# Kernel optimization log

Hardware: AMD Instinct MI355X
Metric: run time of the kernel (lower is better)

Reference implementation:

```python
import jax, jax.numpy as jnp
import numpy as np

F_NODES = 360        # nodes per graph == num_features (square connectome)
NUM_GRAPHS = 128
NUM_EDGES = 1_000_000
C = 128              # hidden_channels
NUM_LAYERS = 3
HIDDEN = 512
NUM_CLASSES = 2
EPS = 1e-5


def _bn(x, g, b):
    # BatchNorm1d in training mode: biased batch statistics over the batch dim.
    m = x.mean(axis=0)
    v = x.var(axis=0)
    return (x - m) * jax.lax.rsqrt(v + EPS) * g + b


def _gcn(x, W, b, src, dst):
    # GCNConv: x' = D^{-1/2} (A + I) D^{-1/2} (x W) + b
    N = x.shape[0]
    h = x @ W                                   # [N, C]
    loop = jnp.arange(N, dtype=src.dtype)
    src2 = jnp.concatenate([src, loop])
    dst2 = jnp.concatenate([dst, loop])
    deg = jax.ops.segment_sum(jnp.ones_like(dst2, dtype=h.dtype), dst2, num_segments=N)
    dinv = jnp.where(deg > 0, jax.lax.rsqrt(deg), 0.0)
    norm = dinv[src2] * dinv[dst2]              # [E+N]
    out = jax.ops.segment_sum(h[src2] * norm[:, None], dst2, num_segments=N)
    return out + b


def setup_inputs() -> dict:
    key = jax.random.key(0)
    ks = jax.random.split(key, 16)
    N = NUM_GRAPHS * F_NODES
    x = jax.random.normal(ks[0], (N, F_NODES), jnp.float32)
    # edges confined within each graph
    g = jax.random.randint(ks[1], (NUM_EDGES,), 0, NUM_GRAPHS)
    edge_src = g * F_NODES + jax.random.randint(ks[2], (NUM_EDGES,), 0, F_NODES)
    edge_dst = g * F_NODES + jax.random.randint(ks[3], (NUM_EDGES,), 0, F_NODES)
    batch = jnp.repeat(jnp.arange(NUM_GRAPHS), F_NODES)

    def lin(k, fi, fo):
        s = 1.0 / np.sqrt(fi)
        return jax.random.uniform(k, (fi, fo), jnp.float32, -s, s)

    input_dim = F_NODES * (F_NODES + 1) // 2    # 64980
    input_dim1 = input_dim + C * NUM_LAYERS     # 65364
    H2 = HIDDEN // 2
    params = dict(
        Wc1=lin(ks[4], F_NODES, C), bc1=jnp.zeros((C,), jnp.float32),
        Wc2=lin(ks[5], C, C), bc2=jnp.zeros((C,), jnp.float32),
        Wc3=lin(ks[6], C, C), bc3=jnp.zeros((C,), jnp.float32),
        bn_g=jnp.ones((input_dim,), jnp.float32), bn_b=jnp.zeros((input_dim,), jnp.float32),
        bnh_g=jnp.ones((C * NUM_LAYERS,), jnp.float32), bnh_b=jnp.zeros((C * NUM_LAYERS,), jnp.float32),
        W1=lin(ks[7], input_dim1, HIDDEN), b1=jnp.zeros((HIDDEN,), jnp.float32),
        g1=jnp.ones((HIDDEN,), jnp.float32), be1=jnp.zeros((HIDDEN,), jnp.float32),
        W2=lin(ks[8], HIDDEN, H2), b2=jnp.zeros((H2,), jnp.float32),
        g2=jnp.ones((H2,), jnp.float32), be2=jnp.zeros((H2,), jnp.float32),
        W3=lin(ks[9], H2, H2), b3=jnp.zeros((H2,), jnp.float32),
        g3=jnp.ones((H2,), jnp.float32), be3=jnp.zeros((H2,), jnp.float32),
        W4=lin(ks[10], H2, NUM_CLASSES), b4=jnp.zeros((NUM_CLASSES,), jnp.float32),
    )
    return {"x": x, "edge_src": edge_src, "edge_dst": edge_dst, "batch": batch, **params}


def reference(x, edge_src, edge_dst, batch,
              Wc1, bc1, Wc2, bc2, Wc3, bc3,
              bn_g, bn_b, bnh_g, bnh_b,
              W1, b1, g1, be1, W2, b2, g2, be2, W3, b3, g3, be3, W4, b4):
    N, F = x.shape
    B = N // F                                   # nodes per graph == F
    # stacked GCN convs with tanh
    xs = [x]
    for W, b in ((Wc1, bc1), (Wc2, bc2), (Wc3, bc3)):
        xs.append(jnp.tanh(_gcn(xs[-1], W, b, edge_src, edge_dst)))
    # per-graph upper-triangular gather of the raw connectome (vectorized)
    iu0, iu1 = np.triu_indices(F)
    x0 = xs[0].reshape(B, F, F)[:, iu0, iu1]     # [B, F(F+1)/2]
    x0 = _bn(x0, bn_g, bn_b)
    # per-layer segment-mean pooling over graphs
    cnt = jax.ops.segment_sum(jnp.ones((N,), x.dtype), batch, num_segments=B)
    h = jnp.concatenate(
        [jax.ops.segment_sum(xx, batch, num_segments=B) / cnt[:, None] for xx in xs[1:]],
        axis=1)                                  # [B, C*num_layers]
    h = _bn(h, bnh_g, bnh_b)
    z = jnp.concatenate([x0, h], axis=1)         # [B, input_dim1]
    # MLP head (dropout in eval mode => identity)
    z = jax.nn.relu(_bn(z @ W1 + b1, g1, be1))
    z = jax.nn.relu(_bn(z @ W2 + b2, g2, be2))
    z = jax.nn.relu(_bn(z @ W3 + b3, g3, be3))
    return jax.nn.log_softmax(z @ W4 + b4, axis=1)
```

## Files before the change

### kernel.cpp

```cpp
#include <hip/hip_runtime.h>
#include <hip/hip_bf16.h>
#include <math.h>

#define FN 360
#define NG 128
#define NN 46080
#define CH 128
#define NE 1000000
#define TRI 64980
#define D1 65364
#define ZLD 65376
#define H1 512
#define H2 256
#define EPS 1e-5f
#define NSPLIT 64
#define NB1 720
#define ERNG 4096
#define NR 245
#define NCH 8
#define CROWS 45
#define BCAP 8
#define OVCAP 192
#define OVGCAP 32768
#define NAGG 384

typedef unsigned short u16;
typedef __attribute__((ext_vector_type(8))) short bf16x8;
typedef __attribute__((ext_vector_type(4))) float f32x4;

__device__ __forceinline__ float bf2f(u16 v) {
  union { unsigned u; float f; } x; x.u = ((unsigned)v) << 16; return x.f;
}
__device__ __forceinline__ u16 f2bf(float f) {
  union { float f; unsigned u; } x; x.f = f;
  unsigned r = x.u + 0x7fffu + ((x.u >> 16) & 1u);
  return (u16)(r >> 16);
}
__device__ __forceinline__ bf16x8 bzero8() {
  bf16x8 z;
#pragma unroll
  for (int j = 0; j < 8; j++) z[j] = 0;
  return z;
}

static const size_t Z_OFF    = 0;
static const size_t PART_OFF = 16736256;
static const size_t EBUF_OFF = PART_OFF;
static const size_t CNT_OFF  = PART_OFF + 4014080;
static const size_t OVF_OFF  = CNT_OFF + 1003520;
static const size_t Y1_OFF   = 50290688;
static const size_t A1_OFF   = 50552832;
static const size_t A2_OFF   = 50683904;
static const size_t A3_OFF   = 50749440;
static const size_t DEG_OFF  = 66355200;
static const size_t HP_OFF   = 66539520;
static const size_t OVN_OFF  = 66736128;
static const size_t AB_OFF   = 66740224;
static const size_t PT_OFF   = 99917824;
static const size_t H_OFF    = 111714304;

__device__ __forceinline__ void pt_epilogue(
    u16 (*PST)[72], const f32x4 (*acc)[4], u16* __restrict__ PT,
    int m0blk, int wid, int quad, int l16) {
  int n0w = (wid >> 1) * 64;
  int mh = (wid & 1) * 32;
#pragma unroll
  for (int tm = 0; tm < 2; tm++)
#pragma unroll
    for (int tn = 0; tn < 4; tn++) {
      int col = n0w + tn * 16 + l16;
#pragma unroll
      for (int r = 0; r < 4; r++)
        PST[col][mh + tm * 16 + quad * 4 + r] = f2bf(acc[tm][tn][r]);
    }
  __syncthreads();
  int t = threadIdx.x;
  int col = t >> 1, seg = t & 1;
#pragma unroll
  for (int u = 0; u < 4; u++) {
    int lrl = seg * 32 + u * 8;
    int row = m0blk + lrl;
    int g = row / FN, lr = row - g * FN;
    *(bf16x8*)(PT + ((size_t)g * CH + col) * FN + lr) = *(const bf16x8*)&PST[col][lrl];
  }
}

__global__ __launch_bounds__(256) void k_gemm1bkt(
    const float* __restrict__ X, const float* __restrict__ W,
    u16* __restrict__ PT,
    const int* __restrict__ src, const int* __restrict__ dst,
    float* __restrict__ deg, u16* __restrict__ ebuf, int* __restrict__ cnt,
    int* __restrict__ govn, unsigned* __restrict__ govf) {
  __shared__ __attribute__((aligned(16))) union {
    struct {
      int cur[NG * NCH];
      u16 bins[NG * NCH][BCAP];
      unsigned ovf[OVCAP];
      int ovn, obase;
    } b;
    u16 WT[128][40];
    u16 PST[128][72];
  } sh;
  if (blockIdx.x >= NB1) {
    int r = blockIdx.x - NB1;
    for (int i = threadIdx.x; i < NG * NCH; i += 256) sh.b.cur[i] = 0;
    if (threadIdx.x == 0) sh.b.ovn = 0;
    __syncthreads();
    int base = r * ERNG;
#pragma unroll 4
    for (int it = 0; it < ERNG / 256; it++) {
      int e = base + it * 256 + threadIdx.x;
      if (e < NE) {
        int s = src[e], d = dst[e];
        atomicAdd(&deg[d], 1.0f);
        int g = d / FN;
        int ls = s - g * FN, ld = d - g * FN;
        int ch = ld / CROWS;
        int gc = g * NCH + ch;
        int slot = atomicAdd(&sh.b.cur[gc], 1);
        if (slot < BCAP) {
          sh.b.bins[gc][slot] = (u16)(ls | ((ld - ch * CROWS) << 9));
        } else {
          int o = atomicAdd(&sh.b.ovn, 1);
          if (o < OVCAP) sh.b.ovf[o] = (unsigned)ls | ((unsigned)ld << 9) | ((unsigned)g << 18);
        }
      }
    }
    __syncthreads();
    {
      const f32x4* sb = (const f32x4*)sh.b.bins;
      f32x4* gb = (f32x4*)(ebuf + (size_t)r * (NG * NCH) * BCAP);
      for (int i = threadIdx.x; i < NG * NCH * BCAP / 8; i += 256) gb[i] = sb[i];
    }
    for (int i = threadIdx.x; i < NG * NCH; i += 256) {
      int c = sh.b.cur[i];
      cnt[r * (NG * NCH) + i] = c < BCAP ? c : BCAP;
    }
    if (threadIdx.x == 0) {
      int n = sh.b.ovn < OVCAP ? sh.b.ovn : OVCAP;
      sh.b.obase = atomicAdd(govn, n);
    }
    __syncthreads();
    int n = sh.b.ovn < OVCAP ? sh.b.ovn : OVCAP;
    int ob = sh.b.obase;
    for (int i = threadIdx.x; i < n; i += 256)
      if (ob + i < OVGCAP) govf[ob + i] = sh.b.ovf[i];
    return;
  }
  const int K = FN;
  int wid = threadIdx.x >> 6, lane = threadIdx.x & 63;
  int quad = lane >> 4, l16 = lane & 15;
  int m0blk = blockIdx.x * 64;
  int m0 = m0blk + (wid & 1) * 32;
  int n0w = (wid >> 1) * 64;
  int kl = threadIdx.x >> 3, nseg = (threadIdx.x & 7) * 16;
  f32x4 acc[2][4];
#pragma unroll
  for (int i = 0; i < 2; i++)
#pragma unroll
    for (int j = 0; j < 4; j++) acc[i][j] = (f32x4){0,0,0,0};
  for (int k0 = 0; k0 < K; k0 += 32) {
    __syncthreads();
    int kg = k0 + kl;
    if (kg < K) {
      const float* wrow = W + (size_t)kg * CH + nseg;
      f32x4 w0 = *(const f32x4*)(wrow);
      f32x4 w1 = *(const f32x4*)(wrow + 4);
      f32x4 w2 = *(const f32x4*)(wrow + 8);
      f32x4 w3 = *(const f32x4*)(wrow + 12);
#pragma unroll
      for (int j = 0; j < 4; j++) {
        sh.WT[nseg + j][kl]      = f2bf(w0[j]);
        sh.WT[nseg + 4 + j][kl]  = f2bf(w1[j]);
        sh.WT[nseg + 8 + j][kl]  = f2bf(w2[j]);
        sh.WT[nseg + 12 + j][kl] = f2bf(w3[j]);
      }
    } else {
#pragma unroll
      for (int j = 0; j < 16; j++) sh.WT[nseg + j][kl] = 0;
    }
    __syncthreads();
    int kk = k0 + quad * 8;
    bool kin = kk < K;
    bf16x8 af[2];
#pragma unroll
    for (int tm = 0; tm < 2; tm++) {
      int row = m0 + tm * 16 + l16;
      bf16x8 a = bzero8();
      if (kin) {
        f32x4 va = *(const f32x4*)(X + (size_t)row * K + kk);
        f32x4 vb = *(const f32x4*)(X + (size_t)row * K + kk + 4);
#pragma unroll
        for (int j = 0; j < 4; j++) { a[j] = (short)f2bf(va[j]); a[4 + j] = (short)f2bf(vb[j]); }
      }
      af[tm] = a;
    }
    bf16x8 bfr[4];
#pragma unroll
    for (int tn = 0; tn < 4; tn++)
      bfr[tn] = *(const bf16x8*)&sh.WT[n0w + tn * 16 + l16][quad * 8];
#pragma unroll
    for (int tm = 0; tm < 2; tm++)
#pragma unroll
      for (int tn = 0; tn < 4; tn++)
        acc[tm][tn] = __builtin_amdgcn_mfma_f32_16x16x32_bf16(af[tm], bfr[tn], acc[tm][tn], 0, 0, 0);
  }
  __syncthreads();
  pt_epilogue(sh.PST, acc, PT, m0blk, wid, quad, l16);
}

__global__ __launch_bounds__(256) void k_abuild3(
    const u16* __restrict__ ebuf, const int* __restrict__ cnt,
    const int* __restrict__ govn, const unsigned* __restrict__ govf,
    const float* __restrict__ deg, u16* __restrict__ Ab) {
  __shared__ __attribute__((aligned(16))) float sA[CROWS * FN];
  __shared__ float sdg[FN];
  __shared__ int scnt[NR];
  int g = blockIdx.x >> 3, ch = blockIdx.x & 7;
  int gc = g * NCH + ch;
  int r0 = ch * CROWS;
  for (int i = threadIdx.x; i < CROWS * FN / 4; i += 256) ((f32x4*)sA)[i] = (f32x4){0,0,0,0};
  for (int i = threadIdx.x; i < FN; i += 256) sdg[i] = rsqrtf(deg[g * FN + i] + 1.0f);
  for (int i = threadIdx.x; i < NR; i += 256) scnt[i] = cnt[i * (NG * NCH) + gc];
  __syncthreads();
  for (int idx = threadIdx.x; idx < NR * BCAP; idx += 256) {
    int r = idx >> 3, sl = idx & (BCAP - 1);
    if (sl < scnt[r]) {
      u16 p = ebuf[((size_t)r * (NG * NCH) + gc) * BCAP + sl];
      int ls = p & 511, ldr = (p >> 9) & 63;
      atomicAdd(&sA[ldr * FN + ls], sdg[ls] * sdg[r0 + ldr]);
    }
  }
  int on = *govn; if (on > OVGCAP) on = OVGCAP;
  for (int i = threadIdx.x; i < on; i += 256) {
    unsigned p = govf[i];
    if ((int)(p >> 18) == g) {
      int ld = (p >> 9) & 511, lr = ld - r0;
      if ((unsigned)lr < (unsigned)CROWS) {
        int ls = p & 511;
        atomicAdd(&sA[lr * FN + ls], sdg[ls] * sdg[ld]);
      }
    }
  }
  __syncthreads();
  if (threadIdx.x < CROWS) {
    int l = r0 + threadIdx.x;
    float dv = sdg[l];
    sA[threadIdx.x * FN + l] += dv * dv;
  }
  __syncthreads();
  unsigned* dstu = (unsigned*)(Ab + (size_t)g * FN * FN + (size_t)r0 * FN);
  for (int i = threadIdx.x; i < CROWS * FN / 2; i += 256) {
    unsigned lo = f2bf(sA[2 * i]), hi = f2bf(sA[2 * i + 1]);
    dstu[i] = lo | (hi << 16);
  }
}

template<bool GUARD>
__device__ __forceinline__ void gbig_body(
    const u16* __restrict__ Z, const float* __restrict__ W1f,
    float* __restrict__ part, int s, int n0b) {
  __shared__ __attribute__((aligned(16))) u16 WT[128][40];
  int wid = threadIdx.x >> 6, lane = threadIdx.x & 63;
  int quad = lane >> 4, l16 = lane & 15;
  int m0 = wid * 32;
  int kl = threadIdx.x >> 3, nseg = (threadIdx.x & 7) * 16;
  int kbeg = s * 1024;
  int kend = GUARD ? ((ZLD < kbeg + 1024) ? ZLD : (kbeg + 1024)) : (kbeg + 1024);
  f32x4 acc[2][8];
#pragma unroll
  for (int i = 0; i < 2; i++)
#pragma unroll
    for (int j = 0; j < 8; j++) acc[i][j] = (f32x4){0,0,0,0};
  for (int k0 = kbeg; k0 < kend; k0 += 32) {
    __syncthreads();
    int kg = k0 + kl;
    if (!GUARD || kg < D1) {
      const float* wrow = W1f + (size_t)kg * H1 + n0b + nseg;
      f32x4 w0 = *(const f32x4*)(wrow);
      f32x4 w1 = *(const f32x4*)(wrow + 4);
      f32x4 w2 = *(const f32x4*)(wrow + 8);
      f32x4 w3 = *(const f32x4*)(wrow + 12);
#pragma unroll
      for (int j = 0; j < 4; j++) {
        WT[nseg + j][kl]      = f2bf(w0[j]);
        WT[nseg + 4 + j][kl]  = f2bf(w1[j]);
        WT[nseg + 8 + j][kl]  = f2bf(w2[j]);
        WT[nseg + 12 + j][kl] = f2bf(w3[j]);
      }
    } else {
#pragma unroll
      for (int j = 0; j < 16; j++) WT[nseg + j][kl] = 0;
    }
    __syncthreads();
    int kk = k0 + quad * 8;
    bf16x8 af[2];
#pragma unroll
    for (int tm = 0; tm < 2; tm++) {
      int row = m0 + tm * 16 + l16;
      af[tm] = *(const bf16x8*)(Z + (size_t)row * ZLD + kk);
    }
    bf16x8 bfr[8];
#pragma unroll
    for (int tn = 0; tn < 8; tn++)
      bfr[tn] = *(const bf16x8*)&WT[tn * 16 + l16][quad * 8];
#pragma unroll
    for (int tm = 0; tm < 2; tm++)
#pragma unroll
      for (int tn = 0; tn < 8; tn++)
        acc[tm][tn] = __builtin_amdgcn_mfma_f32_16x16x32_bf16(af[tm], bfr[tn], acc[tm][tn], 0, 0, 0);
  }
#pragma unroll
  for (int tm = 0; tm < 2; tm++)
#pragma unroll
    for (int tn = 0; tn < 8; tn++) {
      int col = n0b + tn * 16 + l16;
      int rowb = m0 + tm * 16 + quad * 4;
#pragma unroll
      for (int r = 0; r < 4; r++)
        part[((size_t)s * NG + rowb + r) * H1 + col] = acc[tm][tn][r];
    }
}

__global__ __launch_bounds__(512) void k_agg(
    const u16* __restrict__ Ab, const u16* __restrict__ PT,
    const float* __restrict__ bias, u16* __restrict__ Hout,
    float* __restrict__ hp, int loff) {
  __shared__ __attribute__((aligned(16))) u16 sA[128][72];
  __shared__ __attribute__((aligned(16))) u16 sP[128][72];
  __shared__ float ps[8][128];
  int id = blockIdx.x;
  int g = (id & 7) + 8 * (id / 24);
  int mb = (id % 24) >> 3;
  int m0blk = mb * 128;
  int t = threadIdx.x;
  int wid = t >> 6, lane = t & 63;
  int quad = lane >> 4, l16 = lane & 15;
  int wr = wid & 1, wc = wid >> 1;
  int mw = wr * 64, nw = wc * 32;
  const u16* Abg = Ab + (size_t)g * FN * FN;
  const u16* PTg = PT + (size_t)g * CH * FN;
  f32x4 acc[4][2];
#pragma unroll
  for (int i = 0; i < 4; i++)
#pragma unroll
    for (int j = 0; j < 2; j++) acc[i][j] = (f32x4){0,0,0,0};
  bf16x8 ra[2], rp[2];
#define AGG_LOAD(k0)                                                          \
  {                                                                           \
    _Pragma("unroll")                                                         \
    for (int i = 0; i < 2; i++) {                                             \
      int lin = i * 512 + t;                                                  \
      int row = lin >> 3, q = lin & 7;                                        \
      int kg = (k0) + q * 8;                                                  \
      int grow = m0blk + row;                                                 \
      ra[i] = (kg < FN && grow < FN)                                          \
                  ? *(const bf16x8*)(Abg + (size_t)grow * FN + kg) : bzero8();\
      rp[i] = (kg < FN)                                                       \
                  ? *(const bf16x8*)(PTg + (size_t)row * FN + kg) : bzero8(); \
    }                                                                         \
  }
  AGG_LOAD(0)
  for (int step = 0; step < 6; step++) {
    __syncthreads();
#pragma unroll
    for (int i = 0; i < 2; i++) {
      int lin = i * 512 + t;
      int row = lin >> 3, q = lin & 7;
      *(bf16x8*)&sA[row][q * 8] = ra[i];
      *(bf16x8*)&sP[row][q * 8] = rp[i];
    }
    __syncthreads();
    if (step < 5) AGG_LOAD((step + 1) * 64)
#pragma unroll
    for (int sub = 0; sub < 2; sub++) {
      bf16x8 af[4], bp[2];
#pragma unroll
      for (int tm = 0; tm < 4; tm++)
        af[tm] = *(const bf16x8*)&sA[mw + tm * 16 + l16][sub * 32 + quad * 8];
#pragma unroll
      for (int tn = 0; tn < 2; tn++)
        bp[tn] = *(const bf16x8*)&sP[nw + tn * 16 + l16][sub * 32 + quad * 8];
#pragma unroll
      for (int tm = 0; tm < 4; tm++)
#pragma unroll
        for (int tn = 0; tn < 2; tn++)
          acc[tm][tn] = __builtin_amdgcn_mfma_f32_16x16x32_bf16(af[tm], bp[tn], acc[tm][tn], 0, 0, 0);
    }
  }
#undef AGG_LOAD
  float lsum[2] = {0.f, 0.f};
#pragma unroll
  for (int tm = 0; tm < 4; tm++)
#pragma unroll
    for (int tn = 0; tn < 2; tn++) {
      int col = nw + tn * 16 + l16;
      float bc = bias[col];
      int rowb = m0blk + mw + tm * 16 + quad * 4;
#pragma unroll
      for (int r = 0; r < 4; r++) {
        int row = rowb + r;
        if (row < FN) {
          float tt = tanhf(acc[tm][tn][r] + bc);
          if (Hout) Hout[(size_t)(g * FN + row) * CH + col] = f2bf(tt);
          lsum[tn] += tt;
        }
      }
    }
  int cid = wr * 4 + quad;
#pragma unroll
  for (int tn = 0; tn < 2; tn++) ps[cid][nw + tn * 16 + l16] = lsum[tn];
  __syncthreads();
  if (t < 128) {
    float s = 0.f;
#pragma unroll
    for (int c = 0; c < 8; c++) s += ps[c][t];
    atomicAdd(&hp[g * 384 + loff + t], s);
  }
}

__global__ __launch_bounds__(256) void k_gemm_xw_bf16(
    const u16* __restrict__ X, const float* __restrict__ W,
    u16* __restrict__ PT,
    const u16* __restrict__ Z, const float* __restrict__ W1f,
    float* __restrict__ part) {
  if (blockIdx.x >= NB1) {
    int id2 = blockIdx.x - NB1;
    gbig_body<false>(Z, W1f, part, id2 >> 2, (id2 & 3) * 128);
    return;
  }
  __shared__ __attribute__((aligned(16))) union { u16 WT[128][40]; u16 PST[128][72]; } sh;
  int wid = threadIdx.x >> 6, lane = threadIdx.x & 63;
  int quad = lane >> 4, l16 = lane & 15;
  int m0blk = blockIdx.x * 64;
  int m0 = m0blk + (wid & 1) * 32;
  int n0w = (wid >> 1) * 64;
  int kl = threadIdx.x >> 3, nseg = (threadIdx.x & 7) * 16;
  f32x4 acc[2][4];
#pragma unroll
  for (int i = 0; i < 2; i++)
#pragma unroll
    for (int j = 0; j < 4; j++) acc[i][j] = (f32x4){0,0,0,0};
  for (int k0 = 0; k0 < CH; k0 += 32) {
    __syncthreads();
    int kg = k0 + kl;
    const float* wrow = W + (size_t)kg * CH + nseg;
    f32x4 w0 = *(const f32x4*)(wrow);
    f32x4 w1 = *(const f32x4*)(wrow + 4);
    f32x4 w2 = *(const f32x4*)(wrow + 8);
    f32x4 w3 = *(const f32x4*)(wrow + 12);
#pragma unroll
    for (int j = 0; j < 4; j++) {
      sh.WT[nseg + j][kl]      = f2bf(w0[j]);
      sh.WT[nseg + 4 + j][kl]  = f2bf(w1[j]);
      sh.WT[nseg + 8 + j][kl]  = f2bf(w2[j]);
      sh.WT[nseg + 12 + j][kl] = f2bf(w3[j]);
    }
    __syncthreads();
    int kk = k0 + quad * 8;
    bf16x8 af[2];
#pragma unroll
    for (int tm = 0; tm < 2; tm++) {
      int row = m0 + tm * 16 + l16;
      af[tm] = *(const bf16x8*)(X + (size_t)row * CH + kk);
    }
    bf16x8 bfr[4];
#pragma unroll
    for (int tn = 0; tn < 4; tn++)
      bfr[tn] = *(const bf16x8*)&sh.WT[n0w + tn * 16 + l16][quad * 8];
#pragma unroll
    for (int tm = 0; tm < 2; tm++)
#pragma unroll
      for (int tn = 0; tn < 4; tn++)
        acc[tm][tn] = __builtin_amdgcn_mfma_f32_16x16x32_bf16(af[tm], bfr[tn], acc[tm][tn], 0, 0, 0);
  }
  __syncthreads();
  pt_epilogue(sh.PST, acc, PT, m0blk, wid, quad, l16);
}

__global__ __launch_bounds__(256) void k_gemm2tri(
    const u16* __restrict__ X, const float* __restrict__ W,
    u16* __restrict__ PT,
    const float* __restrict__ x, const float* __restrict__ gam,
    const float* __restrict__ bet, u16* __restrict__ z) {
  if (blockIdx.x >= NB1) {
    int i = blockIdx.x - NB1;
    int off = i * FN - (i * (i - 1)) / 2;
    for (int j = i + (int)threadIdx.x; j < FN; j += 256) {
      float s = 0.f, ss = 0.f;
#pragma unroll 8
      for (int b = 0; b < NG; b++) {
        float v = x[(size_t)(b * FN + i) * FN + j];
        s += v; ss += v * v;
      }
      float mean = s * (1.0f / NG);
      float var = fmaxf(ss * (1.0f / NG) - mean * mean, 0.f);
      float rstd = rsqrtf(var + EPS);
      int f = off + (j - i);
      float ga = gam[f] * rstd;
      float bb = bet[f] - mean * ga;
#pragma unroll 8
      for (int b = 0; b < NG; b++) {
        float v = x[(size_t)(b * FN + i) * FN + j];
        z[(size_t)b * ZLD + f] = f2bf(v * ga + bb);
      }
    }
    return;
  }
  __shared__ __attribute__((aligned(16))) union { u16 WT[128][40]; u16 PST[128][72]; } sh;
  int wid = threadIdx.x >> 6, lane = threadIdx.x & 63;
  int quad = lane >> 4, l16 = lane & 15;
  int m0blk = blockIdx.x * 64;
  int m0 = m0blk + (wid & 1) * 32;
  int n0w = (wid >> 1) * 64;
  int kl = threadIdx.x >> 3, nseg = (threadIdx.x & 7) * 16;
  f32x4 acc[2][4];
#pragma unroll
  for (int i = 0; i < 2; i++)
#pragma unroll
    for (int j = 0; j < 4; j++) acc[i][j] = (f32x4){0,0,0,0};
  for (int k0 = 0; k0 < CH; k0 += 32) {
    __syncthreads();
    int kg = k0 + kl;
    const float* wrow = W + (size_t)kg * CH + nseg;
    f32x4 w0 = *(const f32x4*)(wrow);
    f32x4 w1 = *(const f32x4*)(wrow + 4);
    f32x4 w2 = *(const f32x4*)(wrow + 8);
    f32x4 w3 = *(const f32x4*)(wrow + 12);
#pragma unroll
    for (int j = 0; j < 4; j++) {
      sh.WT[nseg + j][kl]      = f2bf(w0[j]);
      sh.WT[nseg + 4 + j][kl]  = f2bf(w1[j]);
      sh.WT[nseg + 8 + j][kl]  = f2bf(w2[j]);
      sh.WT[nseg + 12 + j][kl] = f2bf(w3[j]);
    }
    __syncthreads();
    int kk = k0 + quad * 8;
    bf16x8 af[2];
#pragma unroll
    for (int tm = 0; tm < 2; tm++) {
      int row = m0 + tm * 16 + l16;
      af[tm] = *(const bf16x8*)(X + (size_t)row * CH + kk);
    }
    bf16x8 bfr[4];
#pragma unroll
    for (int tn = 0; tn < 4; tn++)
      bfr[tn] = *(const bf16x8*)&sh.WT[n0w + tn * 16 + l16][quad * 8];
#pragma unroll
    for (int tm = 0; tm < 2; tm++)
#pragma unroll
      for (int tn = 0; tn < 4; tn++)
        acc[tm][tn] = __builtin_amdgcn_mfma_f32_16x16x32_bf16(af[tm], bfr[tn], acc[tm][tn], 0, 0, 0);
  }
  __syncthreads();
  pt_epilogue(sh.PST, acc, PT, m0blk, wid, quad, l16);
}

__global__ void k_hpbn(const float* __restrict__ hp,
                       const float* __restrict__ hgam, const float* __restrict__ hbet,
                       u16* __restrict__ z) {
  for (int c = threadIdx.x; c < 384; c += 256) {
    float s = 0.f, ss = 0.f;
#pragma unroll 8
    for (int m = 0; m < NG; m++) {
      float v = hp[m * 384 + c] * (1.0f / FN);
      s += v; ss += v * v;
    }
    float mean = s * (1.0f / NG);
    float var = fmaxf(ss * (1.0f / NG) - mean * mean, 0.f);
    float rstd = rsqrtf(var + EPS);
    float ga = hgam[c] * rstd;
    float bb = hbet[c] - mean * ga;
#pragma unroll 8
    for (int m = 0; m < NG; m++)
      z[(size_t)m * ZLD + TRI + c] = f2bf(hp[m * 384 + c] * (1.0f / FN) * ga + bb);
  }
  if (threadIdx.x < NG) {
    for (int t = 0; t < ZLD - D1; t++)
      z[(size_t)threadIdx.x * ZLD + D1 + t] = 0;
  }
}

__global__ __launch_bounds__(256) void k_gbig_tail(
    const u16* __restrict__ Z, const float* __restrict__ W1f, float* __restrict__ part) {
  gbig_body<true>(Z, W1f, part, NSPLIT - 1, blockIdx.x * 128);
}

__global__ void k_red(const float* __restrict__ part, float* __restrict__ y1) {
  int idx = blockIdx.x * 256 + threadIdx.x;
  float s = 0.f;
#pragma unroll 8
  for (int i = 0; i < NSPLIT; i++) s += part[(size_t)i * 65536 + idx];
  y1[idx] = s;
}

__global__ __launch_bounds__(256) void k_bnrelu(
    const float* __restrict__ y, const float* __restrict__ gam,
    const float* __restrict__ bet, u16* __restrict__ a, int N) {
  __shared__ float sb[4][64], sb2[4][64];
  int c63 = threadIdx.x & 63;
  int grp = threadIdx.x >> 6;
  int c = blockIdx.x * 64 + c63;
  float s = 0.f, ss = 0.f;
#pragma unroll 8
  for (int m = grp * 32; m < grp * 32 + 32; m++) {
    float v = y[(size_t)m * N + c]; s += v; ss += v * v;
  }
  sb[grp][c63] = s; sb2[grp][c63] = ss;
  __syncthreads();
  float S = sb[0][c63] + sb[1][c63] + sb[2][c63] + sb[3][c63];
  float SS = sb2[0][c63] + sb2[1][c63] + sb2[2][c63] + sb2[3][c63];
  float mean = S * (1.0f / NG);
  float var = fmaxf(SS * (1.0f / NG) - mean * mean, 0.f);
  float rstd = rsqrtf(var + EPS);
  float ga = gam[c] * rstd;
  float bb = bet[c] - mean * ga;
#pragma unroll 8
  for (int m = grp * 32; m < grp * 32 + 32; m++) {
    float v = y[(size_t)m * N + c] * ga + bb;
    a[(size_t)m * N + c] = f2bf(fmaxf(v, 0.f));
  }
}

__global__ __launch_bounds__(256) void k_mlpbn(
    const u16* __restrict__ A, const float* __restrict__ W,
    const float* __restrict__ gam, const float* __restrict__ bet,
    u16* __restrict__ aout, int K, int N) {
  __shared__ __attribute__((aligned(16))) u16 WT[64][40];
  __shared__ float rs[4][4][4][16], rss[4][4][4][16];
  int wid = threadIdx.x >> 6, lane = threadIdx.x & 63;
  int quad = lane >> 4, l16 = lane & 15;
  int n0b = blockIdx.x * 64;
  int m0 = wid * 32;
  int kl = threadIdx.x >> 3;
  int nseg = (threadIdx.x & 7) * 8;
  f32x4 acc[2][4];
#pragma unroll
  for (int i = 0; i < 2; i++)
#pragma unroll
    for (int j = 0; j < 4; j++) acc[i][j] = (f32x4){0,0,0,0};
  for (int k0 = 0; k0 < K; k0 += 32) {
    __syncthreads();
    const float* wrow = W + (size_t)(k0 + kl) * N + n0b + nseg;
    f32x4 w0 = *(const f32x4*)(wrow);
    f32x4 w1 = *(const f32x4*)(wrow + 4);
#pragma unroll
    for (int j = 0; j < 4; j++) {
      WT[nseg + j][kl]     = f2bf(w0[j]);
      WT[nseg + 4 + j][kl] = f2bf(w1[j]);
    }
    __syncthreads();
    int kk = k0 + quad * 8;
    bf16x8 af[2];
#pragma unroll
    for (int tm = 0; tm < 2; tm++) {
      int row = m0 + tm * 16 + l16;
      af[tm] = *(const bf16x8*)(A + (size_t)row * K + kk);
    }
    bf16x8 bfr[4];
#pragma unroll
    for (int tn = 0; tn < 4; tn++)
      bfr[tn] = *(const bf16x8*)&WT[tn * 16 + l16][quad * 8];
#pragma unroll
    for (int tm = 0; tm < 2; tm++)
#pragma unroll
      for (int tn = 0; tn < 4; tn++)
        acc[tm][tn] = __builtin_amdgcn_mfma_f32_16x16x32_bf16(af[tm], bfr[tn], acc[tm][tn], 0, 0, 0);
  }
  __syncthreads();
#pragma unroll
  for (int tn = 0; tn < 4; tn++) {
    float s = 0.f, ss = 0.f;
#pragma unroll
    for (int tm = 0; tm < 2; tm++)
#pragma unroll
      for (int r = 0; r < 4; r++) { float v = acc[tm][tn][r]; s += v; ss += v * v; }
    rs[wid][quad][tn][l16] = s;
    rss[wid][quad][tn][l16] = ss;
  }
  __syncthreads();
#pragma unroll
  for (int tn = 0; tn < 4; tn++) {
    float S = 0.f, SS = 0.f;
#pragma unroll
    for (int w = 0; w < 4; w++)
#pragma unroll
      for (int q = 0; q < 4; q++) { S += rs[w][q][tn][l16]; SS += rss[w][q][tn][l16]; }
    float mean = S * (1.0f / NG);
    float var = fmaxf(SS * (1.0f / NG) - mean * mean, 0.f);
    float rstd = rsqrtf(var + EPS);
    int col = n0b + tn * 16 + l16;
    float ga = gam[col] * rstd;
    float bb = bet[col] - mean * ga;
#pragma unroll
    for (int tm = 0; tm < 2; tm++) {
      int rowb = m0 + tm * 16 + quad * 4;
#pragma unroll
      for (int r = 0; r < 4; r++) {
        float v = acc[tm][tn][r] * ga + bb;
        aout[(size_t)(rowb + r) * N + col] = f2bf(fmaxf(v, 0.f));
      }
    }
  }
}

__global__ void k_head(const u16* __restrict__ a3, const float* __restrict__ W4,
                       const float* __restrict__ b4, float* __restrict__ out) {
  __shared__ float w4s[H2 * 2];
  int m = threadIdx.x;
  for (int i = m; i < H2 * 2; i += 128) w4s[i] = W4[i];
  __syncthreads();
  float a0 = b4[0], a1 = b4[1];
  for (int k0 = 0; k0 < H2; k0 += 8) {
    bf16x8 v = *(const bf16x8*)(a3 + (size_t)m * H2 + k0);
#pragma unroll
    for (int j = 0; j < 8; j++) {
      float f = bf2f((u16)v[j]);
      a0 += f * w4s[(k0 + j) * 2];
      a1 += f * w4s[(k0 + j) * 2 + 1];
    }
  }
  float mx = fmaxf(a0, a1);
  float lse = mx + logf(expf(a0 - mx) + expf(a1 - mx));
  out[m * 2]     = a0 - lse;
  out[m * 2 + 1] = a1 - lse;
}

extern "C" void kernel_launch(void* const* d_in, const int* in_sizes, int n_in,
                              void* d_out, int out_size, void* d_ws, size_t ws_size,
                              hipStream_t stream) {
  const float* x    = (const float*)d_in[0];
  const int* esrc   = (const int*)d_in[1];
  const int* edst   = (const int*)d_in[2];
  const float* Wc1 = (const float*)d_in[4];  const float* bc1 = (const float*)d_in[5];
  const float* Wc2 = (const float*)d_in[6];  const float* bc2 = (const float*)d_in[7];
  const float* Wc3 = (const float*)d_in[8];  const float* bc3 = (const float*)d_in[9];
  const float* bn_g = (const float*)d_in[10]; const float* bn_b = (const float*)d_in[11];
  const float* bnh_g = (const float*)d_in[12]; const float* bnh_b = (const float*)d_in[13];
  const float* W1 = (const float*)d_in[14];
  const float* g1 = (const float*)d_in[16]; const float* be1 = (const float*)d_in[17];
  const float* W2 = (const float*)d_in[18];
  const float* g2 = (const float*)d_in[20]; const float* be2 = (const float*)d_in[21];
  const float* W3 = (const float*)d_in[22];
  const float* g3 = (const float*)d_in[24]; const float* be3 = (const float*)d_in[25];
  const float* W4 = (const float*)d_in[26]; const float* b4 = (const float*)d_in[27];

  char* ws = (char*)d_ws;
  float* deg  = (float*)(ws + DEG_OFF);
  float* hp   = (float*)(ws + HP_OFF);
  int*   govn = (int*)(ws + OVN_OFF);
  u16*   Ab   = (u16*)(ws + AB_OFF);
  u16*   ebuf = (u16*)(ws + EBUF_OFF);
  int*   cnt  = (int*)(ws + CNT_OFF);
  unsigned* govf = (unsigned*)(ws + OVF_OFF);
  u16*   PT   = (u16*)(ws + PT_OFF);
  u16*   h    = (u16*)(ws + H_OFF);
  u16*   z    = (u16*)(ws + Z_OFF);
  float* part = (float*)(ws + PART_OFF);
  float* y1   = (float*)(ws + Y1_OFF);
  u16*   a1   = (u16*)(ws + A1_OFF);
  u16*   a2   = (u16*)(ws + A2_OFF);
  u16*   a3   = (u16*)(ws + A3_OFF);

  (void)hipMemsetAsync(deg, 0, (size_t)NN * 4 + (size_t)NG * 384 * 4 + 4, stream);

  dim3 b256(256);
  dim3 b512(512);
  k_gemm1bkt<<<dim3(NB1 + NR), b256, 0, stream>>>(x, Wc1, PT, esrc, edst, deg, ebuf, cnt, govn, govf);
  k_abuild3<<<dim3(NG * NCH), b256, 0, stream>>>(ebuf, cnt, govn, govf, deg, Ab);
  k_agg<<<dim3(NAGG), b512, 0, stream>>>(Ab, PT, bc1, h, hp, 0);
  k_gemm2tri<<<dim3(NB1 + FN), b256, 0, stream>>>(h, Wc2, PT, x, bn_g, bn_b, z);
  k_agg<<<dim3(NAGG), b512, 0, stream>>>(Ab, PT, bc2, h, hp, CH);
  k_gemm_xw_bf16<<<dim3(NB1 + 252), b256, 0, stream>>>(h, Wc3, PT, z, W1, part);
  k_agg<<<dim3(NAGG), b512, 0, stream>>>(Ab, PT, bc3, (u16*)nullptr, hp, 2 * CH);
  k_hpbn<<<dim3(1), b256, 0, stream>>>(hp, bnh_g, bnh_b, z);
  k_gbig_tail<<<dim3(4), b256, 0, stream>>>(z, W1, part);
  k_red<<<dim3(65536 / 256), b256, 0, stream>>>(part, y1);
  k_bnrelu<<<dim3(H1 / 64), b256, 0, stream>>>(y1, g1, be1, a1, H1);
  k_mlpbn<<<dim3(H2 / 64), b256, 0, stream>>>(a1, W2, g2, be2, a2, H1, H2);
  k_mlpbn<<<dim3(H2 / 64), b256, 0, stream>>>(a2, W3, g3, be3, a3, H2, H2);
  k_head<<<dim3(1), dim3(128), 0, stream>>>(a3, W4, b4, (float*)d_out);
}
```

Before: 620.6 us.

## Spread big W1 GEMM chunks across agg launches and prefetch weight tiles

The 252 big-GEMM (W1) split-K blocks, previously all packed into one launch alongside the third feature GEMM, are now split into three groups of 84. Two groups ride as extra blocks on the second and third aggregation launches, and one stays with the feature GEMM, so the heavy W1 streaming overlaps more kernels. The gbig body is templated for 256 or 512 threads and register-prefetches the next W and Z slice before the MFMA step. Weight-tile loads in several GEMMs switch from 16-float vector chunks to strided scalar loads, changing the LDS write pattern. This adds register pressure and relies on the agg launches having spare occupancy.

```diff
diff --git a/kernel.cpp b/kernel.cpp
--- a/kernel.cpp
+++ b/kernel.cpp
@@ -23,6 +23,7 @@
 #define OVCAP 192
 #define OVGCAP 32768
 #define NAGG 384
+#define NRID 84
 
 typedef unsigned short u16;
 typedef __attribute__((ext_vector_type(8))) short bf16x8;
@@ -83,6 +84,88 @@
     int g = row / FN, lr = row - g * FN;
     *(bf16x8*)(PT + ((size_t)g * CH + col) * FN + lr) = *(const bf16x8*)&PST[col][lrl];
   }
+}
+
+template<int NT, bool GUARD>
+__device__ __forceinline__ void gbig_body(
+    const u16* __restrict__ Z, const float* __restrict__ W1f,
+    float* __restrict__ part, int s, int n0b) {
+  __shared__ __attribute__((aligned(16))) u16 WT[128][40];
+  constexpr int TM = (NT == 256) ? 2 : 1;
+  constexpr int NJ = (NT == 256) ? 16 : 8;
+  constexpr int NSTR = (NT == 256) ? 8 : 16;
+  int t = threadIdx.x;
+  int wid = t >> 6, lane = t & 63;
+  int quad = lane >> 4, l16 = lane & 15;
+  int m0 = wid * (TM * 16);
+  int kl = (NT == 256) ? (t >> 3) : (t >> 4);
+  int nb = (NT == 256) ? (t & 7) : (t & 15);
+  int kbeg = s * 1024;
+  int kend = GUARD ? ((ZLD < kbeg + 1024) ? ZLD : (kbeg + 1024)) : (kbeg + 1024);
+  f32x4 acc[TM][8];
+#pragma unroll
+  for (int i = 0; i < TM; i++)
+#pragma unroll
+    for (int j = 0; j < 8; j++) acc[i][j] = (f32x4){0,0,0,0};
+  float wreg[NJ];
+  bf16x8 zreg[TM];
+  {
+    int kg = kbeg + kl;
+    if (!GUARD || kg < D1) {
+      const float* wr = W1f + (size_t)kg * H1 + n0b + nb;
+#pragma unroll
+      for (int j = 0; j < NJ; j++) wreg[j] = wr[j * NSTR];
+    } else {
+#pragma unroll
+      for (int j = 0; j < NJ; j++) wreg[j] = 0.f;
+    }
+#pragma unroll
+    for (int tm = 0; tm < TM; tm++)
+      zreg[tm] = *(const bf16x8*)(Z + (size_t)(m0 + tm * 16 + l16) * ZLD + kbeg + quad * 8);
+  }
+  for (int k0 = kbeg; k0 < kend; k0 += 32) {
+    __syncthreads();
+#pragma unroll
+    for (int j = 0; j < NJ; j++)
+      WT[nb + j * NSTR][kl] = f2bf(wreg[j]);
+    bf16x8 az[TM];
+#pragma unroll
+    for (int tm = 0; tm < TM; tm++) az[tm] = zreg[tm];
+    __syncthreads();
+    if (k0 + 32 < kend) {
+      int kg = k0 + 32 + kl;
+      if (!GUARD || kg < D1) {
+        const float* wr = W1f + (size_t)kg * H1 + n0b + nb;
+#pragma unroll
+        for (int j = 0; j < NJ; j++) wreg[j] = wr[j * NSTR];
+      } else {
+#pragma unroll
+        for (int j = 0; j < NJ; j++) wreg[j] = 0.f;
+      }
+#pragma unroll
+      for (int tm = 0; tm < TM; tm++)
+        zreg[tm] = *(const bf16x8*)(Z + (size_t)(m0 + tm * 16 + l16) * ZLD + k0 + 32 + quad * 8);
+    }
+    bf16x8 bfr[8];
+#pragma unroll
+    for (int tn = 0; tn < 8; tn++)
+      bfr[tn] = *(const bf16x8*)&WT[tn * 16 + l16][quad * 8];
+#pragma unroll
+    for (int tm = 0; tm < TM; tm++)
+#pragma unroll
+      for (int tn = 0; tn < 8; tn++)
+        acc[tm][tn] = __builtin_amdgcn_mfma_f32_16x16x32_bf16(az[tm], bfr[tn], acc[tm][tn], 0, 0, 0);
+  }
+#pragma unroll
+  for (int tm = 0; tm < TM; tm++)
+#pragma unroll
+    for (int tn = 0; tn < 8; tn++) {
+      int col = n0b + tn * 16 + l16;
+      int rowb = m0 + tm * 16 + quad * 4;
+#pragma unroll
+      for (int r = 0; r < 4; r++)
+        part[((size_t)s * NG + rowb + r) * H1 + col] = acc[tm][tn][r];
+    }
 }
 
 __global__ __launch_bounds__(256) void k_gemm1bkt(
@@ -153,7 +236,7 @@
   int m0blk = blockIdx.x * 64;
   int m0 = m0blk + (wid & 1) * 32;
   int n0w = (wid >> 1) * 64;
-  int kl = threadIdx.x >> 3, nseg = (threadIdx.x & 7) * 16;
+  int kl = threadIdx.x >> 3, nb = threadIdx.x & 7;
   f32x4 acc[2][4];
 #pragma unroll
   for (int i = 0; i < 2; i++)
@@ -163,21 +246,12 @@
     __syncthreads();
     int kg = k0 + kl;
     if (kg < K) {
-      const float* wrow = W + (size_t)kg * CH + nseg;
-      f32x4 w0 = *(const f32x4*)(wrow);
-      f32x4 w1 = *(const f32x4*)(wrow + 4);
-      f32x4 w2 = *(const f32x4*)(wrow + 8);
-      f32x4 w3 = *(const f32x4*)(wrow + 12);
-#pragma unroll
-      for (int j = 0; j < 4; j++) {
-        sh.WT[nseg + j][kl]      = f2bf(w0[j]);
-        sh.WT[nseg + 4 + j][kl]  = f2bf(w1[j]);
-        sh.WT[nseg + 8 + j][kl]  = f2bf(w2[j]);
-        sh.WT[nseg + 12 + j][kl] = f2bf(w3[j]);
-      }
+      const float* wr = W + (size_t)kg * CH + nb;
+#pragma unroll
+      for (int j = 0; j < 16; j++) sh.WT[nb + 8 * j][kl] = f2bf(wr[8 * j]);
     } else {
 #pragma unroll
-      for (int j = 0; j < 16; j++) sh.WT[nseg + j][kl] = 0;
+      for (int j = 0; j < 16; j++) sh.WT[nb + 8 * j][kl] = 0;
     }
     __syncthreads();
     int kk = k0 + quad * 8;
@@ -256,76 +330,17 @@
   }
 }
 
-template<bool GUARD>
-__device__ __forceinline__ void gbig_body(
-    const u16* __restrict__ Z, const float* __restrict__ W1f,
-    float* __restrict__ part, int s, int n0b) {
-  __shared__ __attribute__((aligned(16))) u16 WT[128][40];
-  int wid = threadIdx.x >> 6, lane = threadIdx.x & 63;
-  int quad = lane >> 4, l16 = lane & 15;
-  int m0 = wid * 32;
-  int kl = threadIdx.x >> 3, nseg = (threadIdx.x & 7) * 16;
-  int kbeg = s * 1024;
-  int kend = GUARD ? ((ZLD < kbeg + 1024) ? ZLD : (kbeg + 1024)) : (kbeg + 1024);
-  f32x4 acc[2][8];
-#pragma unroll
-  for (int i = 0; i < 2; i++)
-#pragma unroll
-    for (int j = 0; j < 8; j++) acc[i][j] = (f32x4){0,0,0,0};
-  for (int k0 = kbeg; k0 < kend; k0 += 32) {
-    __syncthreads();
-    int kg = k0 + kl;
-    if (!GUARD || kg < D1) {
-      const float* wrow = W1f + (size_t)kg * H1 + n0b + nseg;
-      f32x4 w0 = *(const f32x4*)(wrow);
-      f32x4 w1 = *(const f32x4*)(wrow + 4);
-      f32x4 w2 = *(const f32x4*)(wrow + 8);
-      f32x4 w3 = *(const f32x4*)(wrow + 12);
-#pragma unroll
-      for (int j = 0; j < 4; j++) {
-        WT[nseg + j][kl]      = f2bf(w0[j]);
-        WT[nseg + 4 + j][kl]  = f2bf(w1[j]);
-        WT[nseg + 8 + j][kl]  = f2bf(w2[j]);
-        WT[nseg + 12 + j][kl] = f2bf(w3[j]);
-      }
-    } else {
-#pragma unroll
-      for (int j = 0; j < 16; j++) WT[nseg + j][kl] = 0;
-    }
-    __syncthreads();
-    int kk = k0 + quad * 8;
-    bf16x8 af[2];
-#pragma unroll
-    for (int tm = 0; tm < 2; tm++) {
-      int row = m0 + tm * 16 + l16;
-      af[tm] = *(const bf16x8*)(Z + (size_t)row * ZLD + kk);
-    }
-    bf16x8 bfr[8];
-#pragma unroll
-    for (int tn = 0; tn < 8; tn++)
-      bfr[tn] = *(const bf16x8*)&WT[tn * 16 + l16][quad * 8];
-#pragma unroll
-    for (int tm = 0; tm < 2; tm++)
-#pragma unroll
-      for (int tn = 0; tn < 8; tn++)
-        acc[tm][tn] = __builtin_amdgcn_mfma_f32_16x16x32_bf16(af[tm], bfr[tn], acc[tm][tn], 0, 0, 0);
-  }
-#pragma unroll
-  for (int tm = 0; tm < 2; tm++)
-#pragma unroll
-    for (int tn = 0; tn < 8; tn++) {
-      int col = n0b + tn * 16 + l16;
-      int rowb = m0 + tm * 16 + quad * 4;
-#pragma unroll
-      for (int r = 0; r < 4; r++)
-        part[((size_t)s * NG + rowb + r) * H1 + col] = acc[tm][tn][r];
-    }
-}
-
 __global__ __launch_bounds__(512) void k_agg(
     const u16* __restrict__ Ab, const u16* __restrict__ PT,
     const float* __restrict__ bias, u16* __restrict__ Hout,
-    float* __restrict__ hp, int loff) {
+    float* __restrict__ hp, int loff,
+    const u16* __restrict__ Z, const float* __restrict__ W1f,
+    float* __restrict__ part, int rbase) {
+  if (blockIdx.x >= NAGG) {
+    int id2 = rbase + (blockIdx.x - NAGG);
+    gbig_body<512, false>(Z, W1f, part, id2 >> 2, (id2 & 3) * 128);
+    return;
+  }
   __shared__ __attribute__((aligned(16))) u16 sA[128][72];
   __shared__ __attribute__((aligned(16))) u16 sP[128][72];
   __shared__ float ps[8][128];
@@ -423,10 +438,10 @@
     const u16* __restrict__ X, const float* __restrict__ W,
     u16* __restrict__ PT,
     const u16* __restrict__ Z, const float* __restrict__ W1f,
-    float* __restrict__ part) {
+    float* __restrict__ part, int rbase) {
   if (blockIdx.x >= NB1) {
-    int id2 = blockIdx.x - NB1;
-    gbig_body<false>(Z, W1f, part, id2 >> 2, (id2 & 3) * 128);
+    int id2 = rbase + (blockIdx.x - NB1);
+    gbig_body<256, false>(Z, W1f, part, id2 >> 2, (id2 & 3) * 128);
     return;
   }
   __shared__ __attribute__((aligned(16))) union { u16 WT[128][40]; u16 PST[128][72]; } sh;
@@ -435,7 +450,7 @@
   int m0blk = blockIdx.x * 64;
   int m0 = m0blk + (wid & 1) * 32;
   int n0w = (wid >> 1) * 64;
-  int kl = threadIdx.x >> 3, nseg = (threadIdx.x & 7) * 16;
+  int kl = threadIdx.x >> 3, nb = threadIdx.x & 7;
   f32x4 acc[2][4];
 #pragma unroll
   for (int i = 0; i < 2; i++)
@@ -444,18 +459,9 @@
   for (int k0 = 0; k0 < CH; k0 += 32) {
     __syncthreads();
     int kg = k0 + kl;
-    const float* wrow = W + (size_t)kg * CH + nseg;
-    f32x4 w0 = *(const f32x4*)(wrow);
-    f32x4 w1 = *(const f32x4*)(wrow + 4);
-    f32x4 w2 = *(const f32x4*)(wrow + 8);
-    f32x4 w3 = *(const f32x4*)(wrow + 12);
-#pragma unroll
-    for (int j = 0; j < 4; j++) {
-      sh.WT[nseg + j][kl]      = f2bf(w0[j]);
-      sh.WT[nseg + 4 + j][kl]  = f2bf(w1[j]);
-      sh.WT[nseg + 8 + j][kl]  = f2bf(w2[j]);
-      sh.WT[nseg + 12 + j][kl] = f2bf(w3[j]);
-    }
+    const float* wr = W + (size_t)kg * CH + nb;
+#pragma unroll
+    for (int j = 0; j < 16; j++) sh.WT[nb + 8 * j][kl] = f2bf(wr[8 * j]);
     __syncthreads();
     int kk = k0 + quad * 8;
     bf16x8 af[2];
@@ -513,7 +519,7 @@
   int m0blk = blockIdx.x * 64;
   int m0 = m0blk + (wid & 1) * 32;
   int n0w = (wid >> 1) * 64;
-  int kl = threadIdx.x >> 3, nseg = (threadIdx.x & 7) * 16;
+  int kl = threadIdx.x >> 3, nb = threadIdx.x & 7;
   f32x4 acc[2][4];
 #pragma unroll
   for (int i = 0; i < 2; i++)
@@ -522,18 +528,9 @@
   for (int k0 = 0; k0 < CH; k0 += 32) {
     __syncthreads();
     int kg = k0 + kl;
-    const float* wrow = W + (size_t)kg * CH + nseg;
-    f32x4 w0 = *(const f32x4*)(wrow);
-    f32x4 w1 = *(const f32x4*)(wrow + 4);
-    f32x4 w2 = *(const f32x4*)(wrow + 8);
-    f32x4 w3 = *(const f32x4*)(wrow + 12);
-#pragma unroll
-    for (int j = 0; j < 4; j++) {
-      sh.WT[nseg + j][kl]      = f2bf(w0[j]);
-      sh.WT[nseg + 4 + j][kl]  = f2bf(w1[j]);
-      sh.WT[nseg + 8 + j][kl]  = f2bf(w2[j]);
-      sh.WT[nseg + 12 + j][kl] = f2bf(w3[j]);
-    }
+    const float* wr = W + (size_t)kg * CH + nb;
+#pragma unroll
+    for (int j = 0; j < 16; j++) sh.WT[nb + 8 * j][kl] = f2bf(wr[8 * j]);
     __syncthreads();
     int kk = k0 + quad * 8;
     bf16x8 af[2];
@@ -583,7 +580,7 @@
 
 __global__ __launch_bounds__(256) void k_gbig_tail(
     const u16* __restrict__ Z, const float* __restrict__ W1f, float* __restrict__ part) {
-  gbig_body<true>(Z, W1f, part, NSPLIT - 1, blockIdx.x * 128);
+  gbig_body<256, true>(Z, W1f, part, NSPLIT - 1, blockIdx.x * 128);
 }
 
 __global__ void k_red(const float* __restrict__ part, float* __restrict__ y1) {
@@ -633,7 +630,7 @@
   int n0b = blockIdx.x * 64;
   int m0 = wid * 32;
   int kl = threadIdx.x >> 3;
-  int nseg = (threadIdx.x & 7) * 8;
+  int nb = threadIdx.x & 7;
   f32x4 acc[2][4];
 #pragma unroll
   for (int i = 0; i < 2; i++)
@@ -641,14 +638,9 @@
     for (int j = 0; j < 4; j++) acc[i][j] = (f32x4){0,0,0,0};
   for (int k0 = 0; k0 < K; k0 += 32) {
     __syncthreads();
-    const float* wrow = W + (size_t)(k0 + kl) * N + n0b + nseg;
-    f32x4 w0 = *(const f32x4*)(wrow);
-    f32x4 w1 = *(const f32x4*)(wrow + 4);
-#pragma unroll
-    for (int j = 0; j < 4; j++) {
-      WT[nseg + j][kl]     = f2bf(w0[j]);
-      WT[nseg + 4 + j][kl] = f2bf(w1[j]);
-    }
+    const float* wr = W + (size_t)(k0 + kl) * N + n0b + nb;
+#pragma unroll
+    for (int j = 0; j < 8; j++) WT[nb + 8 * j][kl] = f2bf(wr[8 * j]);
     __syncthreads();
     int kk = k0 + quad * 8;
     bf16x8 af[2];
@@ -768,11 +760,11 @@
   dim3 b512(512);
   k_gemm1bkt<<<dim3(NB1 + NR), b256, 0, stream>>>(x, Wc1, PT, esrc, edst, deg, ebuf, cnt, govn, govf);
   k_abuild3<<<dim3(NG * NCH), b256, 0, stream>>>(ebuf, cnt, govn, govf, deg, Ab);
-  k_agg<<<dim3(NAGG), b512, 0, stream>>>(Ab, PT, bc1, h, hp, 0);
+  k_agg<<<dim3(NAGG), b512, 0, stream>>>(Ab, PT, bc1, h, hp, 0, z, W1, part, 0);
   k_gemm2tri<<<dim3(NB1 + FN), b256, 0, stream>>>(h, Wc2, PT, x, bn_g, bn_b, z);
-  k_agg<<<dim3(NAGG), b512, 0, stream>>>(Ab, PT, bc2, h, hp, CH);
-  k_gemm_xw_bf16<<<dim3(NB1 + 252), b256, 0, stream>>>(h, Wc3, PT, z, W1, part);
-  k_agg<<<dim3(NAGG), b512, 0, stream>>>(Ab, PT, bc3, (u16*)nullptr, hp, 2 * CH);
+  k_agg<<<dim3(NAGG + NRID), b512, 0, stream>>>(Ab, PT, bc2, h, hp, CH, z, W1, part, 0);
+  k_gemm_xw_bf16<<<dim3(NB1 + NRID), b256, 0, stream>>>(h, Wc3, PT, z, W1, part, NRID);
+  k_agg<<<dim3(NAGG + NRID), b512, 0, stream>>>(Ab, PT, bc3, (u16*)nullptr, hp, 2 * CH, z, W1, part, 2 * NRID);
   k_hpbn<<<dim3(1), b256, 0, stream>>>(hp, bnh_g, bnh_b, z);
   k_gbig_tail<<<dim3(4), b256, 0, stream>>>(z, W1, part);
   k_red<<<dim3(65536 / 256), b256, 0, stream>>>(part, y1);
```

Measured after the change: 654.6 us. 5.5% more time.
